# Optimization experiments

Measured on AMD Instinct MI355X. Metric: run time of the kernel, lower is better.

The kernel has to match this reference:

```python
import jax, jax.numpy as jnp
import numpy as np
from jax import tree_util

H = 64; V = 64; INNER = 32; STEPS = 3
LR = 0.05; B1 = 0.9; B2 = 0.999; EPS = 1e-8
B = 256; L = 2048


def setup_inputs() -> dict:
    key = jax.random.key(0)
    ks = jax.random.split(key, 8)
    def rn(k, shape, s):
        return jax.random.normal(k, shape, jnp.float32) * s
    return dict(
        seq=jax.random.randint(ks[0], (B, L), 0, V),
        emb=rn(ks[1], (V, H), 0.02),
        ff_w1=rn(ks[2], (2 * H, H), (1.0 / H) ** 0.5), ff_b1=jnp.zeros((2 * H,), jnp.float32),
        ff_w2=rn(ks[3], (H, 2 * H), (1.0 / (2 * H)) ** 0.5), ff_b2=jnp.zeros((H,), jnp.float32),
        ln_g=jnp.ones((H,), jnp.float32), ln_b=jnp.zeros((H,), jnp.float32),
        fc1_w=rn(ks[4], (INNER, H), (1.0 / H) ** 0.5), fc1_b=jnp.zeros((INNER,), jnp.float32),
        fc2_w=rn(ks[5], (H, INNER), (1.0 / INNER) ** 0.5), fc2_b=jnp.zeros((H,), jnp.float32),
        out_w=rn(ks[6], (V, H), (1.0 / H) ** 0.5), out_b=jnp.zeros((V,), jnp.float32),
    )


def _inner_loss(params, k, v):
    w1, b1, w2, b2 = params
    pred = jnp.maximum(k @ w1.T + b1, 0.0) @ w2.T + b2
    return jnp.mean((pred - v) ** 2)


def reference(seq, emb, ff_w1, ff_b1, ff_w2, ff_b2, ln_g, ln_b,
              fc1_w, fc1_b, fc2_w, fc2_b, out_w, out_b):
    # Encoder: embed -> FFN residual -> LayerNorm
    e = emb[seq]                                             # [B, L, H]
    ff = jnp.maximum(e @ ff_w1.T + ff_b1, 0.0) @ ff_w2.T + ff_b2
    x = e + ff
    mu = x.mean(-1, keepdims=True)
    var = ((x - mu) ** 2).mean(-1, keepdims=True)
    hs = (x - mu) / jnp.sqrt(var + 1e-5) * ln_g + ln_b       # [B, L, H]

    # Torch detaches hs / params inside the inner loop, so no grad flows there.
    hs_d = jax.lax.stop_gradient(hs)
    ts = np.arange(0, L - 3, 2)                              # T = 1023 steps per pass
    kh = jnp.tile(hs_d[:, ts], (1, STEPS, 1))                # [B, STEPS*T, H]
    vh = jnp.tile(hs_d[:, ts + 1], (1, STEPS, 1))
    qh = hs_d[:, -1]                                         # [B, H]
    p0 = tuple(jax.lax.stop_gradient(p) for p in (fc1_w, fc1_b, fc2_w, fc2_b))

    def run_one(khs, vhs, q):
        zeros = tuple(jnp.zeros_like(p) for p in p0)

        def step(carry, kv):
            params, m1, m2, n = carry
            k, v = kv
            g = jax.grad(_inner_loss)(params, k, v)
            n1 = n + 1.0
            c1 = 1.0 - B1 ** n1
            c2 = 1.0 - B2 ** n1
            m1n = tree_util.tree_map(lambda m, gg: B1 * m + (1 - B1) * gg, m1, g)
            m2n = tree_util.tree_map(lambda m, gg: B2 * m + (1 - B2) * gg * gg, m2, g)
            pn = tree_util.tree_map(
                lambda p, a, b: p - LR * (a / c1) / (jnp.sqrt(b / c2) + EPS),
                params, m1n, m2n)
            return (pn, m1n, m2n, n1), None

        (pf, _, _, _), _ = jax.lax.scan(step, (p0, zeros, zeros, jnp.float32(0.0)), (khs, vhs))
        w1, b1, w2, b2 = pf
        return jnp.maximum(q @ w1.T + b1, 0.0) @ w2.T + b2

    ctxs = jax.vmap(run_one)(kh, vh, qh)                     # [B, H]
    return ctxs @ out_w.T + out_b                            # [B, V]
```

## Files before the change

### kernel.cpp

```cpp
#include <hip/hip_runtime.h>


template <int CTRL>
__device__ __forceinline__ float dpp_add(float x) {
  union { float f; int i; } u, r;
  u.f = x;
  r.i = __builtin_amdgcn_update_dpp(0, u.i, CTRL, 0xF, 0xF, true);
  return x + r.f;
}

__device__ __forceinline__ float swz16_add(float x) {
  union { float f; int i; } u, r;
  u.f = x;
  r.i = __builtin_amdgcn_ds_swizzle(u.i, 0x401F);
  return x + r.f;
}

__device__ __forceinline__ float bp_add(float x, int idx) {
  union { float f; int i; } u, r;
  u.f = x;
  r.i = __builtin_amdgcn_ds_bpermute(idx, u.i);
  return x + r.f;
}

__device__ __forceinline__ void adam_upd(float& p, float& m1, float& m2,
                                         float g, float c2inv, float nls)
{
  m1 = fmaf(0.9f,  m1, 0.1f   * g);
  m2 = fmaf(0.999f, m2, 0.001f * (g * g));
  float den = __builtin_amdgcn_sqrtf(m2 * c2inv) + 1e-8f;
  p = fmaf(nls * m1, __builtin_amdgcn_rcpf(den), p);
}

__global__ void prep_kernel(const float* __restrict__ emb,
                            const float* __restrict__ ffw1, const float* __restrict__ ffb1,
                            const float* __restrict__ ffw2, const float* __restrict__ ffb2,
                            const float* __restrict__ lng,  const float* __restrict__ lnb,
                            float* __restrict__ hs_out)
{
  const int v = blockIdx.x;
  const int t = threadIdx.x;
  __shared__ float e[64];
  __shared__ float r[128];
  if (t < 64) e[t] = emb[v * 64 + t];
  __syncthreads();
  {
    float s = ffb1[t];
    const float* wrow = ffw1 + t * 64;
#pragma unroll 8
    for (int m = 0; m < 64; ++m) s = fmaf(wrow[m], e[m], s);
    r[t] = fmaxf(s, 0.f);
  }
  __syncthreads();
  if (t < 64) {
    float s = ffb2[t];
    const float* wrow = ffw2 + t * 128;
#pragma unroll 8
    for (int o = 0; o < 128; ++o) s = fmaf(wrow[o], r[o], s);
    float x = e[t] + s;
    float mu = x;
    for (int m = 1; m < 64; m <<= 1) mu += __shfl_xor(mu, m, 64);
    mu *= (1.f / 64.f);
    float dv = x - mu;
    float var = dv * dv;
    for (int m = 1; m < 64; m <<= 1) var += __shfl_xor(var, m, 64);
    var *= (1.f / 64.f);
    float hs = dv / sqrtf(var + 1e-5f);
    hs_out[v * 64 + t] = hs * lng[t] + lnb[t];
  }
}

__global__ __launch_bounds__(64)
void table_kernel(float* __restrict__ tab)
{
  if (threadIdx.x != 0) return;
  double pb1 = 1.0, pb2 = 1.0;
  for (int n = 0; n < 3069; ++n) {
    pb1 *= 0.9; pb2 *= 0.999;
    float c1inv = __builtin_amdgcn_rcpf((float)(1.0 - pb1));
    float c2inv = __builtin_amdgcn_rcpf((float)(1.0 - pb2));
    tab[2 * n]     = -0.05f * c1inv;
    tab[2 * n + 1] = c2inv;
  }
}

__global__ __launch_bounds__(256)
void scan_kernel(const int* __restrict__ seq, const float* __restrict__ hs_tab,
                 const float* __restrict__ tab_g,
                 const float* __restrict__ fc1w, const float* __restrict__ fc1b,
                 const float* __restrict__ fc2w, const float* __restrict__ fc2b,
                 const float* __restrict__ outw, const float* __restrict__ outb,
                 float* __restrict__ out)
{
  const int b    = blockIdx.x;
  const int t    = threadIdx.x;
  const int lane = t & 63;
  const int wv   = t >> 6;
  const int i1   = t >> 3;
  const int j0   = (t & 7) << 3;
  const int p0   = i1 << 1;
  const int c0   = (t & 7) << 2;
  const int sub  = t & 7;
  const int bp32 = ((lane ^ 32) << 2);

  __shared__ __align__(16) float hs[4096];
  __shared__ __align__(16) int   sq[2048];
  __shared__ __align__(16) float tabs[6144];
  __shared__ __align__(16) float h_s[32];
  __shared__ __align__(16) float dhp[32][4];
  __shared__ __align__(16) float ctx[64];

  for (int i = t; i < 1024; i += 256)
    ((float4*)hs)[i] = ((const float4*)hs_tab)[i];
  {
    const int4* sg = (const int4*)(seq + (long long)b * 2048);
    for (int i = t; i < 512; i += 256) ((int4*)sq)[i] = sg[i];
  }
  for (int i = t; i < 1536; i += 256)
    ((float4*)tabs)[i] = ((const float4*)tab_g)[i];

  float w1r[8], m1a[8], m2a[8];
  float w2r[8], m1b[8], m2b[8];
#pragma unroll
  for (int jj = 0; jj < 8; ++jj) {
    w1r[jj] = fc1w[i1 * 64 + j0 + jj];
    m1a[jj] = 0.f; m2a[jj] = 0.f;
  }
#pragma unroll
  for (int z = 0; z < 8; ++z) {
    w2r[z] = fc2w[(p0 + (z >> 2)) * 32 + c0 + (z & 3)];
    m1b[z] = 0.f; m2b[z] = 0.f;
  }
  float b1v  = fc1b[i1];     float m1c = 0.f, m2c = 0.f;
  float b2v0 = fc2b[p0];     float m1d0 = 0.f, m2d0 = 0.f;
  float b2v1 = fc2b[p0 + 1]; float m1d1 = 0.f, m2d1 = 0.f;

  __syncthreads();

  int jm = 1;

  float nls_c  = tabs[0];
  float c2i_c  = tabs[1];
  float kk[8], hv, v0, v1;
  {
    const int ka = sq[0], vb = sq[1];
    const float4 k0 = *(const float4*)(hs + ka * 64 + j0);
    const float4 k1 = *(const float4*)(hs + ka * 64 + j0 + 4);
    kk[0]=k0.x; kk[1]=k0.y; kk[2]=k0.z; kk[3]=k0.w;
    kk[4]=k1.x; kk[5]=k1.y; kk[6]=k1.z; kk[7]=k1.w;
    v0 = hs[vb * 64 + p0];
    v1 = hs[vb * 64 + p0 + 1];
    float pa = 0.f;
#pragma unroll
    for (int jj = 0; jj < 8; ++jj) pa = fmaf(w1r[jj], kk[jj], pa);
    pa = dpp_add<0xB1>(pa);
    pa = dpp_add<0x4E>(pa);
    pa = dpp_add<0x141>(pa);
    hv = fmaxf(pa + b1v, 0.f);
    if (sub == 1) h_s[i1] = hv;
  }
  __syncthreads();

  for (int step = 0; step < 3069; ++step) {
    const int ni = (step < 3068) ? (step + 1) : 3068;
    const float nls_n = tabs[2 * ni];
    const float c2i_n = tabs[2 * ni + 1];
    const float nls   = nls_c;
    const float c2inv = c2i_c;

    float kn[8], v0n, v1n;
    {
      int ka, vb;
      if (step < 3068) {
        ka = sq[2 * jm]; vb = sq[2 * jm + 1];
        jm = (jm == 1022) ? 0 : jm + 1;
      } else {
        ka = sq[2047]; vb = 0;
      }
      const float4 k0 = *(const float4*)(hs + ka * 64 + j0);
      const float4 k1 = *(const float4*)(hs + ka * 64 + j0 + 4);
      kn[0]=k0.x; kn[1]=k0.y; kn[2]=k0.z; kn[3]=k0.w;
      kn[4]=k1.x; kn[5]=k1.y; kn[6]=k1.z; kn[7]=k1.w;
      v0n = hs[vb * 64 + p0];
      v1n = hs[vb * 64 + p0 + 1];
    }

    float hh[4];
    {
      const float4 h4 = *(const float4*)(h_s + c0);
      hh[0]=h4.x; hh[1]=h4.y; hh[2]=h4.z; hh[3]=h4.w;
    }
    float q0 = 0.f, q1 = 0.f;
#pragma unroll
    for (int ii = 0; ii < 4; ++ii) {
      q0 = fmaf(w2r[ii],     hh[ii], q0);
      q1 = fmaf(w2r[4 + ii], hh[ii], q1);
    }
    q0 = dpp_add<0xB1>(q0);   q1 = dpp_add<0xB1>(q1);
    q0 = dpp_add<0x4E>(q0);   q1 = dpp_add<0x4E>(q1);
    q0 = dpp_add<0x141>(q0);  q1 = dpp_add<0x141>(q1);
    const float dd0 = 0.03125f * (q0 + b2v0 - v0);
    const float dd1 = 0.03125f * (q1 + b2v1 - v1);

    float dp[4];
#pragma unroll
    for (int ii = 0; ii < 4; ++ii)
      dp[ii] = fmaf(w2r[4 + ii], dd1, w2r[ii] * dd0);

#pragma unroll
    for (int ii = 0; ii < 4; ++ii) dp[ii] = dpp_add<0x128>(dp[ii]);
#pragma unroll
    for (int ii = 0; ii < 4; ++ii) dp[ii] = swz16_add(dp[ii]);
#pragma unroll
    for (int ii = 0; ii < 4; ++ii) dp[ii] = bp_add(dp[ii], bp32);
    if (lane < 8) {
      dhp[4 * lane + 0][wv] = dp[0];
      dhp[4 * lane + 1][wv] = dp[1];
      dhp[4 * lane + 2][wv] = dp[2];
      dhp[4 * lane + 3][wv] = dp[3];
    }

#pragma unroll
    for (int ii = 0; ii < 4; ++ii) {
      adam_upd(w2r[ii],     m1b[ii],     m2b[ii],     dd0 * hh[ii], c2inv, nls);
      adam_upd(w2r[4 + ii], m1b[4 + ii], m2b[4 + ii], dd1 * hh[ii], c2inv, nls);
    }
    adam_upd(b2v0, m1d0, m2d0, dd0, c2inv, nls);
    adam_upd(b2v1, m1d1, m2d1, dd1, c2inv, nls);
    __syncthreads();

    const float4 d4 = *(const float4*)dhp[i1];
    const float dhsum = (d4.x + d4.y) + (d4.z + d4.w);
    const float dh = (hv > 0.f) ? dhsum : 0.f;
#pragma unroll
    for (int jj = 0; jj < 8; ++jj)
      adam_upd(w1r[jj], m1a[jj], m2a[jj], dh * kk[jj], c2inv, nls);
    adam_upd(b1v, m1c, m2c, dh, c2inv, nls);

    {
#pragma unroll
      for (int jj = 0; jj < 8; ++jj) kk[jj] = kn[jj];
      v0 = v0n; v1 = v1n;
      float pa = 0.f;
#pragma unroll
      for (int jj = 0; jj < 8; ++jj) pa = fmaf(w1r[jj], kk[jj], pa);
      pa = dpp_add<0xB1>(pa);
      pa = dpp_add<0x4E>(pa);
      pa = dpp_add<0x141>(pa);
      hv = fmaxf(pa + b1v, 0.f);
      if (sub == 1) h_s[i1] = hv;
    }
    nls_c = nls_n;
    c2i_c = c2i_n;
    __syncthreads();
  }

  {
    float hh[4];
    const float4 h4 = *(const float4*)(h_s + c0);
    hh[0]=h4.x; hh[1]=h4.y; hh[2]=h4.z; hh[3]=h4.w;
    float q0 = 0.f, q1 = 0.f;
#pragma unroll
    for (int ii = 0; ii < 4; ++ii) {
      q0 = fmaf(w2r[ii],     hh[ii], q0);
      q1 = fmaf(w2r[4 + ii], hh[ii], q1);
    }
    q0 = dpp_add<0xB1>(q0);   q1 = dpp_add<0xB1>(q1);
    q0 = dpp_add<0x4E>(q0);   q1 = dpp_add<0x4E>(q1);
    q0 = dpp_add<0x141>(q0);  q1 = dpp_add<0x141>(q1);
    if (sub == 2) { ctx[p0] = q0 + b2v0; ctx[p0 + 1] = q1 + b2v1; }
  }
  __syncthreads();

  if (t < 64) {
    float acc = outb[t];
    const float* wrow = outw + t * 64;
#pragma unroll 8
    for (int p = 0; p < 64; ++p) acc = fmaf(wrow[p], ctx[p], acc);
    out[(long long)b * 64 + t] = acc;
  }
}

extern "C" void kernel_launch(void* const* d_in, const int* in_sizes, int n_in,
                              void* d_out, int out_size, void* d_ws, size_t ws_size,
                              hipStream_t stream) {
  const int*   seq  = (const int*)  d_in[0];
  const float* emb  = (const float*)d_in[1];
  const float* ffw1 = (const float*)d_in[2];
  const float* ffb1 = (const float*)d_in[3];
  const float* ffw2 = (const float*)d_in[4];
  const float* ffb2 = (const float*)d_in[5];
  const float* lng  = (const float*)d_in[6];
  const float* lnb  = (const float*)d_in[7];
  const float* fc1w = (const float*)d_in[8];
  const float* fc1b = (const float*)d_in[9];
  const float* fc2w = (const float*)d_in[10];
  const float* fc2b = (const float*)d_in[11];
  const float* outw = (const float*)d_in[12];
  const float* outb = (const float*)d_in[13];
  float* out    = (float*)d_out;
  float* hs_tab = (float*)d_ws;
  float* tab    = (float*)d_ws + 4096;

  prep_kernel<<<64, 128, 0, stream>>>(emb, ffw1, ffb1, ffw2, ffb2, lng, lnb, hs_tab);
  table_kernel<<<1, 64, 0, stream>>>(tab);
  scan_kernel<<<256, 256, 0, stream>>>(seq, hs_tab, tab, fc1w, fc1b, fc2w, fc2b,
                                       outw, outb, out);
}
```

Baseline: 2.582 ms.

## Split scan block into separate fc2 and fc1 warp groups with 512 threads

The scan kernel now launches 512 threads per batch row. The first 256 threads own the fc2 weights and compute the output error and its backprop, and the other 256 own the fc1 weights and do the hidden-layer update and next forward. The cross-wave reduction of the hidden gradient drops the swizzle and bpermute stages and instead writes 16 partial sums per hidden unit to shared memory, which the fc1 threads sum. The aim is to shorten each step's serial dependency chain and raise parallelism per step, at the cost of divergent branches, double the waves per CU, and more shared-memory reads.

```diff
diff --git a/kernel.cpp b/kernel.cpp
--- a/kernel.cpp
+++ b/kernel.cpp
@@ -6,20 +6,6 @@
   union { float f; int i; } u, r;
   u.f = x;
   r.i = __builtin_amdgcn_update_dpp(0, u.i, CTRL, 0xF, 0xF, true);
-  return x + r.f;
-}
-
-__device__ __forceinline__ float swz16_add(float x) {
-  union { float f; int i; } u, r;
-  u.f = x;
-  r.i = __builtin_amdgcn_ds_swizzle(u.i, 0x401F);
-  return x + r.f;
-}
-
-__device__ __forceinline__ float bp_add(float x, int idx) {
-  union { float f; int i; } u, r;
-  u.f = x;
-  r.i = __builtin_amdgcn_ds_bpermute(idx, u.i);
   return x + r.f;
 }
 
@@ -84,7 +70,7 @@
   }
 }
 
-__global__ __launch_bounds__(256)
+__global__ __launch_bounds__(512)
 void scan_kernel(const int* __restrict__ seq, const float* __restrict__ hs_tab,
                  const float* __restrict__ tab_g,
                  const float* __restrict__ fc1w, const float* __restrict__ fc1b,
@@ -92,64 +78,67 @@
                  const float* __restrict__ outw, const float* __restrict__ outb,
                  float* __restrict__ out)
 {
-  const int b    = blockIdx.x;
-  const int t    = threadIdx.x;
-  const int lane = t & 63;
-  const int wv   = t >> 6;
-  const int i1   = t >> 3;
-  const int j0   = (t & 7) << 3;
-  const int p0   = i1 << 1;
-  const int c0   = (t & 7) << 2;
-  const int sub  = t & 7;
-  const int bp32 = ((lane ^ 32) << 2);
+  const int b      = blockIdx.x;
+  const int t      = threadIdx.x;
+  const bool isw2  = (t < 256);
+  const int tl     = t & 255;
+  const int lane   = tl & 63;
+  const int wv     = tl >> 6;
+  const int i1     = tl >> 3;
+  const int j0     = (tl & 7) << 3;
+  const int p0     = i1 << 1;
+  const int c0     = (tl & 7) << 2;
+  const int sub    = tl & 7;
 
   __shared__ __align__(16) float hs[4096];
   __shared__ __align__(16) int   sq[2048];
   __shared__ __align__(16) float tabs[6144];
   __shared__ __align__(16) float h_s[32];
-  __shared__ __align__(16) float dhp[32][4];
+  __shared__ __align__(16) float dhp[32][20];
   __shared__ __align__(16) float ctx[64];
 
-  for (int i = t; i < 1024; i += 256)
+  for (int i = t; i < 1024; i += 512)
     ((float4*)hs)[i] = ((const float4*)hs_tab)[i];
   {
     const int4* sg = (const int4*)(seq + (long long)b * 2048);
-    for (int i = t; i < 512; i += 256) ((int4*)sq)[i] = sg[i];
-  }
-  for (int i = t; i < 1536; i += 256)
+    ((int4*)sq)[t] = sg[t];
+  }
+  for (int i = t; i < 1536; i += 512)
     ((float4*)tabs)[i] = ((const float4*)tab_g)[i];
 
   float w1r[8], m1a[8], m2a[8];
+  float b1v = 0.f, m1c = 0.f, m2c = 0.f;
   float w2r[8], m1b[8], m2b[8];
-#pragma unroll
-  for (int jj = 0; jj < 8; ++jj) {
-    w1r[jj] = fc1w[i1 * 64 + j0 + jj];
-    m1a[jj] = 0.f; m2a[jj] = 0.f;
-  }
-#pragma unroll
-  for (int z = 0; z < 8; ++z) {
-    w2r[z] = fc2w[(p0 + (z >> 2)) * 32 + c0 + (z & 3)];
-    m1b[z] = 0.f; m2b[z] = 0.f;
-  }
-  float b1v  = fc1b[i1];     float m1c = 0.f, m2c = 0.f;
-  float b2v0 = fc2b[p0];     float m1d0 = 0.f, m2d0 = 0.f;
-  float b2v1 = fc2b[p0 + 1]; float m1d1 = 0.f, m2d1 = 0.f;
+  float b2v0 = 0.f, m1d0 = 0.f, m2d0 = 0.f;
+  float b2v1 = 0.f, m1d1 = 0.f, m2d1 = 0.f;
+  if (isw2) {
+#pragma unroll
+    for (int z = 0; z < 8; ++z) {
+      w2r[z] = fc2w[(p0 + (z >> 2)) * 32 + c0 + (z & 3)];
+      m1b[z] = 0.f; m2b[z] = 0.f;
+    }
+    b2v0 = fc2b[p0];
+    b2v1 = fc2b[p0 + 1];
+  } else {
+#pragma unroll
+    for (int jj = 0; jj < 8; ++jj) {
+      w1r[jj] = fc1w[i1 * 64 + j0 + jj];
+      m1a[jj] = 0.f; m2a[jj] = 0.f;
+    }
+    b1v = fc1b[i1];
+  }
 
   __syncthreads();
 
   int jm = 1;
-
-  float nls_c  = tabs[0];
-  float c2i_c  = tabs[1];
-  float kk[8], hv, v0, v1;
-  {
-    const int ka = sq[0], vb = sq[1];
+  float kk[8], hv = 0.f, v0 = 0.f, v1 = 0.f;
+
+  if (!isw2) {
+    const int ka = sq[0];
     const float4 k0 = *(const float4*)(hs + ka * 64 + j0);
     const float4 k1 = *(const float4*)(hs + ka * 64 + j0 + 4);
     kk[0]=k0.x; kk[1]=k0.y; kk[2]=k0.z; kk[3]=k0.w;
     kk[4]=k1.x; kk[5]=k1.y; kk[6]=k1.z; kk[7]=k1.w;
-    v0 = hs[vb * 64 + p0];
-    v1 = hs[vb * 64 + p0 + 1];
     float pa = 0.f;
 #pragma unroll
     for (int jj = 0; jj < 8; ++jj) pa = fmaf(w1r[jj], kk[jj], pa);
@@ -158,89 +147,89 @@
     pa = dpp_add<0x141>(pa);
     hv = fmaxf(pa + b1v, 0.f);
     if (sub == 1) h_s[i1] = hv;
+  } else {
+    const int vb = sq[1];
+    v0 = hs[vb * 64 + p0];
+    v1 = hs[vb * 64 + p0 + 1];
   }
   __syncthreads();
 
   for (int step = 0; step < 3069; ++step) {
-    const int ni = (step < 3068) ? (step + 1) : 3068;
-    const float nls_n = tabs[2 * ni];
-    const float c2i_n = tabs[2 * ni + 1];
-    const float nls   = nls_c;
-    const float c2inv = c2i_c;
-
-    float kn[8], v0n, v1n;
-    {
-      int ka, vb;
-      if (step < 3068) {
-        ka = sq[2 * jm]; vb = sq[2 * jm + 1];
-        jm = (jm == 1022) ? 0 : jm + 1;
-      } else {
-        ka = sq[2047]; vb = 0;
+    const float nls   = tabs[2 * step];
+    const float c2inv = tabs[2 * step + 1];
+
+    float kn[8];
+    float hh[4];
+    float dd0 = 0.f, dd1 = 0.f;
+
+    if (isw2) {
+      const float4 h4 = *(const float4*)(h_s + c0);
+      hh[0]=h4.x; hh[1]=h4.y; hh[2]=h4.z; hh[3]=h4.w;
+      float q0 = 0.f, q1 = 0.f;
+#pragma unroll
+      for (int ii = 0; ii < 4; ++ii) {
+        q0 = fmaf(w2r[ii],     hh[ii], q0);
+        q1 = fmaf(w2r[4 + ii], hh[ii], q1);
       }
+      q0 = dpp_add<0xB1>(q0);   q1 = dpp_add<0xB1>(q1);
+      q0 = dpp_add<0x4E>(q0);   q1 = dpp_add<0x4E>(q1);
+      q0 = dpp_add<0x141>(q0);  q1 = dpp_add<0x141>(q1);
+      dd0 = 0.03125f * (q0 + b2v0 - v0);
+      dd1 = 0.03125f * (q1 + b2v1 - v1);
+
+      float dp[4];
+#pragma unroll
+      for (int ii = 0; ii < 4; ++ii)
+        dp[ii] = fmaf(w2r[4 + ii], dd1, w2r[ii] * dd0);
+#pragma unroll
+      for (int ii = 0; ii < 4; ++ii) dp[ii] = dpp_add<0x128>(dp[ii]);
+      if (!(lane & 8)) {
+        const int slot = wv * 4 + (lane >> 4);
+        const int colb = (lane & 7) << 2;
+        dhp[colb + 0][slot] = dp[0];
+        dhp[colb + 1][slot] = dp[1];
+        dhp[colb + 2][slot] = dp[2];
+        dhp[colb + 3][slot] = dp[3];
+      }
+    } else {
+      const int ka = (step < 3068) ? sq[2 * jm] : sq[2047];
       const float4 k0 = *(const float4*)(hs + ka * 64 + j0);
       const float4 k1 = *(const float4*)(hs + ka * 64 + j0 + 4);
       kn[0]=k0.x; kn[1]=k0.y; kn[2]=k0.z; kn[3]=k0.w;
       kn[4]=k1.x; kn[5]=k1.y; kn[6]=k1.z; kn[7]=k1.w;
-      v0n = hs[vb * 64 + p0];
-      v1n = hs[vb * 64 + p0 + 1];
-    }
-
-    float hh[4];
-    {
-      const float4 h4 = *(const float4*)(h_s + c0);
-      hh[0]=h4.x; hh[1]=h4.y; hh[2]=h4.z; hh[3]=h4.w;
-    }
-    float q0 = 0.f, q1 = 0.f;
-#pragma unroll
-    for (int ii = 0; ii < 4; ++ii) {
-      q0 = fmaf(w2r[ii],     hh[ii], q0);
-      q1 = fmaf(w2r[4 + ii], hh[ii], q1);
-    }
-    q0 = dpp_add<0xB1>(q0);   q1 = dpp_add<0xB1>(q1);
-    q0 = dpp_add<0x4E>(q0);   q1 = dpp_add<0x4E>(q1);
-    q0 = dpp_add<0x141>(q0);  q1 = dpp_add<0x141>(q1);
-    const float dd0 = 0.03125f * (q0 + b2v0 - v0);
-    const float dd1 = 0.03125f * (q1 + b2v1 - v1);
-
-    float dp[4];
-#pragma unroll
-    for (int ii = 0; ii < 4; ++ii)
-      dp[ii] = fmaf(w2r[4 + ii], dd1, w2r[ii] * dd0);
-
-#pragma unroll
-    for (int ii = 0; ii < 4; ++ii) dp[ii] = dpp_add<0x128>(dp[ii]);
-#pragma unroll
-    for (int ii = 0; ii < 4; ++ii) dp[ii] = swz16_add(dp[ii]);
-#pragma unroll
-    for (int ii = 0; ii < 4; ++ii) dp[ii] = bp_add(dp[ii], bp32);
-    if (lane < 8) {
-      dhp[4 * lane + 0][wv] = dp[0];
-      dhp[4 * lane + 1][wv] = dp[1];
-      dhp[4 * lane + 2][wv] = dp[2];
-      dhp[4 * lane + 3][wv] = dp[3];
-    }
-
-#pragma unroll
-    for (int ii = 0; ii < 4; ++ii) {
-      adam_upd(w2r[ii],     m1b[ii],     m2b[ii],     dd0 * hh[ii], c2inv, nls);
-      adam_upd(w2r[4 + ii], m1b[4 + ii], m2b[4 + ii], dd1 * hh[ii], c2inv, nls);
-    }
-    adam_upd(b2v0, m1d0, m2d0, dd0, c2inv, nls);
-    adam_upd(b2v1, m1d1, m2d1, dd1, c2inv, nls);
+    }
     __syncthreads();
 
-    const float4 d4 = *(const float4*)dhp[i1];
-    const float dhsum = (d4.x + d4.y) + (d4.z + d4.w);
-    const float dh = (hv > 0.f) ? dhsum : 0.f;
-#pragma unroll
-    for (int jj = 0; jj < 8; ++jj)
-      adam_upd(w1r[jj], m1a[jj], m2a[jj], dh * kk[jj], c2inv, nls);
-    adam_upd(b1v, m1c, m2c, dh, c2inv, nls);
-
-    {
+    if (isw2) {
+#pragma unroll
+      for (int ii = 0; ii < 4; ++ii) {
+        adam_upd(w2r[ii],     m1b[ii],     m2b[ii],     dd0 * hh[ii], c2inv, nls);
+        adam_upd(w2r[4 + ii], m1b[4 + ii], m2b[4 + ii], dd1 * hh[ii], c2inv, nls);
+      }
+      adam_upd(b2v0, m1d0, m2d0, dd0, c2inv, nls);
+      adam_upd(b2v1, m1d1, m2d1, dd1, c2inv, nls);
+      const int vb = (step < 3068) ? sq[2 * jm + 1] : 0;
+      jm = (jm == 1022) ? 0 : jm + 1;
+      v0 = hs[vb * 64 + p0];
+      v1 = hs[vb * 64 + p0 + 1];
+    } else {
+      const float4 pA = *(const float4*)&dhp[i1][0];
+      const float4 pB = *(const float4*)&dhp[i1][4];
+      const float4 pC = *(const float4*)&dhp[i1][8];
+      const float4 pD = *(const float4*)&dhp[i1][12];
+      const float W0 = (pA.x + pA.y) + (pA.z + pA.w);
+      const float W1 = (pB.x + pB.y) + (pB.z + pB.w);
+      const float W2 = (pC.x + pC.y) + (pC.z + pC.w);
+      const float W3 = (pD.x + pD.y) + (pD.z + pD.w);
+      const float dhsum = (W0 + W1) + (W2 + W3);
+      const float dh = (hv > 0.f) ? dhsum : 0.f;
+#pragma unroll
+      for (int jj = 0; jj < 8; ++jj)
+        adam_upd(w1r[jj], m1a[jj], m2a[jj], dh * kk[jj], c2inv, nls);
+      adam_upd(b1v, m1c, m2c, dh, c2inv, nls);
+      jm = (jm == 1022) ? 0 : jm + 1;
 #pragma unroll
       for (int jj = 0; jj < 8; ++jj) kk[jj] = kn[jj];
-      v0 = v0n; v1 = v1n;
       float pa = 0.f;
 #pragma unroll
       for (int jj = 0; jj < 8; ++jj) pa = fmaf(w1r[jj], kk[jj], pa);
@@ -250,21 +239,16 @@
       hv = fmaxf(pa + b1v, 0.f);
       if (sub == 1) h_s[i1] = hv;
     }
-    nls_c = nls_n;
-    c2i_c = c2i_n;
     __syncthreads();
   }
 
-  {
-    float hh[4];
+  if (isw2) {
     const float4 h4 = *(const float4*)(h_s + c0);
-    hh[0]=h4.x; hh[1]=h4.y; hh[2]=h4.z; hh[3]=h4.w;
     float q0 = 0.f, q1 = 0.f;
-#pragma unroll
-    for (int ii = 0; ii < 4; ++ii) {
-      q0 = fmaf(w2r[ii],     hh[ii], q0);
-      q1 = fmaf(w2r[4 + ii], hh[ii], q1);
-    }
+    q0 = fmaf(w2r[0], h4.x, q0); q1 = fmaf(w2r[4], h4.x, q1);
+    q0 = fmaf(w2r[1], h4.y, q0); q1 = fmaf(w2r[5], h4.y, q1);
+    q0 = fmaf(w2r[2], h4.z, q0); q1 = fmaf(w2r[6], h4.z, q1);
+    q0 = fmaf(w2r[3], h4.w, q0); q1 = fmaf(w2r[7], h4.w, q1);
     q0 = dpp_add<0xB1>(q0);   q1 = dpp_add<0xB1>(q1);
     q0 = dpp_add<0x4E>(q0);   q1 = dpp_add<0x4E>(q1);
     q0 = dpp_add<0x141>(q0);  q1 = dpp_add<0x141>(q1);
@@ -304,6 +288,6 @@
 
   prep_kernel<<<64, 128, 0, stream>>>(emb, ffw1, ffb1, ffw2, ffb2, lng, lnb, hs_tab);
   table_kernel<<<1, 64, 0, stream>>>(tab);
-  scan_kernel<<<256, 256, 0, stream>>>(seq, hs_tab, tab, fc1w, fc1b, fc2w, fc2b,
+  scan_kernel<<<256, 512, 0, stream>>>(seq, hs_tab, tab, fc1w, fc1b, fc2w, fc2b,
                                        outw, outb, out);
 }
```

Result: no change. 2.601 ms (+0.7%).
